# Performance work log

Measured on AMD Instinct MI355X. Metric: run time of the kernel, lower is better.

## Reference

```python
import math
import jax, jax.numpy as jnp
import numpy as np

B, S, D, H = 4, 2048, 1024, 16
HD = D // H
NEG = float(jnp.finfo(jnp.float16).min)  # matches torch.finfo(torch.float16).min

def setup_inputs() -> dict:
    key = jax.random.key(0)
    ks = jax.random.split(key, 10)
    s = 1.0 / math.sqrt(D)
    return {
        "x": jax.random.normal(ks[0], (B, S, D), jnp.float32),
        "mask": jax.random.randint(ks[1], (B, 1, S, S), 0, 2).astype(bool),
        "Wq": jax.random.normal(ks[2], (D, D), jnp.float32) * s,
        "bq": jnp.zeros((D,), jnp.float32),
        "Wk": jax.random.normal(ks[3], (D, D), jnp.float32) * s,
        "bk": jnp.zeros((D,), jnp.float32),
        "Wv": jax.random.normal(ks[4], (D, D), jnp.float32) * s,
        "bv": jnp.zeros((D,), jnp.float32),
        "Wf": jax.random.normal(ks[5], (D, D), jnp.float32) * s,
        "bf": jnp.zeros((D,), jnp.float32),
    }

def reference(x, mask, Wq, bq, Wk, bk, Wv, bv, Wf, bf):
    b, s, d = x.shape
    # QKV projections (torch Linear: y = x @ W.T + b)
    q = (x @ Wq.T + bq).reshape(b, s, H, HD).transpose(0, 2, 1, 3)  # [b,h,s,hd]
    k = (x @ Wk.T + bk).reshape(b, s, H, HD).transpose(0, 2, 1, 3)
    v = (x @ Wv.T + bv).reshape(b, s, H, HD).transpose(0, 2, 1, 3)
    scores = jnp.einsum('bhqd,bhkd->bhqk', q, k) / math.sqrt(HD)
    scores = jnp.where(mask, scores, NEG)  # masked_fill_(~mask, fp16 min)
    p = jax.nn.softmax(scores, axis=-1)    # dropout is identity (eval / drop_rate=0)
    h = jnp.einsum('bhqk,bhkd->bhqd', p, v).transpose(0, 2, 1, 3).reshape(b, s, d)
    return h @ Wf.T + bf
```

## Files before the change

### kernel.cpp

```cpp
#include <hip/hip_runtime.h>
#include <math.h>

constexpr int S = 2048, D = 1024, H = 16;
constexpr float QSCL = 0.18033688011112042f;

typedef __attribute__((ext_vector_type(8))) short bf16x8;
typedef __attribute__((ext_vector_type(4))) short s16x4;
typedef __attribute__((ext_vector_type(4))) float f32x4;
typedef __attribute__((ext_vector_type(16))) float f32x16;

#define MFMA16(a,b,c) __builtin_amdgcn_mfma_f32_16x16x32_bf16(a,b,c,0,0,0)
#define MFMA32(a,b,c) __builtin_amdgcn_mfma_f32_32x32x16_bf16(a,b,c,0,0,0)

#define GLDS16(g, l) __builtin_amdgcn_global_load_lds( \
    (const __attribute__((address_space(1))) unsigned*)(const void*)(g), \
    (__attribute__((address_space(3))) unsigned*)(void*)(l), 16, 0, 0)

__device__ inline short f2bf(float f) {
    union { float f; unsigned u; } c; c.f = f;
    unsigned u = c.u + 0x7fffu + ((c.u >> 16) & 1u);
    return (short)(u >> 16);
}

__global__ __launch_bounds__(256)
void conv_pack(const float* __restrict__ x,  const float* __restrict__ wq,
               const float* __restrict__ wk, const float* __restrict__ wv,
               const float* __restrict__ wf,
               short* __restrict__ xb,  short* __restrict__ wqb,
               short* __restrict__ wkb, short* __restrict__ wvb,
               short* __restrict__ wfb)
{
    int i = blockIdx.x * 256 + threadIdx.x;
    const float* s; short* d; int o;
    if (i < 2097152) { s = x; d = xb; o = i; }
    else {
        int j = i - 2097152; int wsel = j >> 18; o = j & 262143;
        s = wsel == 0 ? wq : wsel == 1 ? wk : wsel == 2 ? wv : wf;
        d = wsel == 0 ? wqb : wsel == 1 ? wkb : wsel == 2 ? wvb : wfb;
    }
    float4 v = ((const float4*)s)[o];
    s16x4 r; r.x = f2bf(v.x); r.y = f2bf(v.y); r.z = f2bf(v.z); r.w = f2bf(v.w);
    ((s16x4*)d)[o] = r;
}

__global__ __launch_bounds__(256)
void conv_maskcol(const int* __restrict__ m, unsigned* __restrict__ o)
{
    int gid = blockIdx.x * 256 + threadIdx.x;
    int lane = gid & 63;
    int tile = (gid >> 6) & 31;
    int grp  = (gid >> 11) & 63;
    int bb   = gid >> 17;
    int qrow = grp * 32 + (lane & 31);
    int h = lane >> 5;
    const int* base = m + (size_t)bb * S * S + (size_t)qrow * S + tile * 64 + 4 * h;
    unsigned wbits = 0;
#pragma unroll
    for (int a = 0; a < 8; ++a) {
        int4 v = *(const int4*)(base + 8 * (a & 3) + 32 * (a >> 2));
        wbits |= (v.x != 0 ? 1u : 0u) << (4 * a);
        wbits |= (v.y != 0 ? 1u : 0u) << (4 * a + 1);
        wbits |= (v.z != 0 ? 1u : 0u) << (4 * a + 2);
        wbits |= (v.w != 0 ? 1u : 0u) << (4 * a + 3);
    }
    o[gid] = wbits;
}

__global__ __launch_bounds__(256, 3)
void qkv_mfma(const short* __restrict__ xb, const short* __restrict__ wcat,
              const float* __restrict__ bq, const float* __restrict__ bk,
              const float* __restrict__ bv,
              short* __restrict__ qo, short* __restrict__ ko, short* __restrict__ vto)
{
    __shared__ short As[128 * 64];
    __shared__ short Bs[128 * 64];
    const int t = threadIdx.x, lane = t & 63;
    const int w = __builtin_amdgcn_readfirstlane(t >> 6);
    const int lr = lane & 15, lg = lane >> 4;
    const int wr = w >> 1, wc = w & 1;
    const int m0 = blockIdx.x * 128, n0 = blockIdx.y * 128;

    const int srow = t >> 3;
    const int scol = ((t & 7) ^ (srow & 7)) * 8;
    const short* asrc = xb   + (size_t)(m0 + srow) * 1024 + scol;
    const short* bsrc = wcat + (size_t)(n0 + srow) * 1024 + scol;
    char* aldst = (char*)As + w * 1024;
    char* bldst = (char*)Bs + w * 1024;

    f32x4 z = {0.f, 0.f, 0.f, 0.f};
    f32x4 acc[4][4];
#pragma unroll
    for (int i = 0; i < 4; ++i)
#pragma unroll
        for (int jj = 0; jj < 4; ++jj) acc[i][jj] = z;

    for (int kt = 0; kt < 1024; kt += 64) {
        __syncthreads();
        GLDS16(asrc + kt,             aldst);
        GLDS16(asrc + kt + 32 * 1024, aldst + 4096);
        GLDS16(asrc + kt + 64 * 1024, aldst + 8192);
        GLDS16(asrc + kt + 96 * 1024, aldst + 12288);
        GLDS16(bsrc + kt,             bldst);
        GLDS16(bsrc + kt + 32 * 1024, bldst + 4096);
        GLDS16(bsrc + kt + 64 * 1024, bldst + 8192);
        GLDS16(bsrc + kt + 96 * 1024, bldst + 12288);
        __syncthreads();
#pragma unroll
        for (int ks = 0; ks < 2; ++ks) {
            bf16x8 af[4], bfr[4];
#pragma unroll
            for (int fi = 0; fi < 4; ++fi) {
                const int ra = wr * 64 + fi * 16 + lr;
                af[fi] = *(const bf16x8*)((const char*)As + ra * 128 +
                          ((ks * 64 + lg * 16) ^ ((ra & 7) << 4)));
                const int rb = wc * 64 + fi * 16 + lr;
                bfr[fi] = *(const bf16x8*)((const char*)Bs + rb * 128 +
                          ((ks * 64 + lg * 16) ^ ((rb & 7) << 4)));
            }
#pragma unroll
            for (int fi = 0; fi < 4; ++fi)
#pragma unroll
                for (int fj = 0; fj < 4; ++fj)
                    acc[fi][fj] = MFMA16(af[fi], bfr[fj], acc[fi][fj]);
        }
    }

    const int bb = m0 >> 11;
    const int ssb = (m0 & (S - 1)) + wr * 64 + lg * 4;
    const int mat = n0 >> 10;
    const int nbase = (n0 & 1023) + wc * 64;

    if (mat == 0) {
#pragma unroll
        for (int fj = 0; fj < 4; ++fj) {
            const int nl = nbase + fj * 16 + lr, hh = nl >> 6, hd = nl & 63;
            const float bi = bq[nl];
#pragma unroll
            for (int fi = 0; fi < 4; ++fi)
#pragma unroll
                for (int r = 0; r < 4; ++r)
                    qo[(((size_t)bb * H + hh) * S + ssb + fi * 16 + r) * 64 + hd] =
                        f2bf((acc[fi][fj][r] + bi) * QSCL);
        }
    } else if (mat == 1) {
#pragma unroll
        for (int fj = 0; fj < 4; ++fj) {
            const int nl = nbase + fj * 16 + lr, hh = nl >> 6, hd = nl & 63;
            const float bi = bk[nl];
#pragma unroll
            for (int fi = 0; fi < 4; ++fi)
#pragma unroll
                for (int r = 0; r < 4; ++r)
                    ko[(((size_t)bb * H + hh) * S + ssb + fi * 16 + r) * 64 + hd] =
                        f2bf(acc[fi][fj][r] + bi);
        }
    } else {
#pragma unroll
        for (int fj = 0; fj < 4; ++fj) {
            const int nl = nbase + fj * 16 + lr, hh = nl >> 6, hd = nl & 63;
            const float bi = bv[nl];
#pragma unroll
            for (int fi = 0; fi < 4; ++fi) {
                s16x4 pk;
#pragma unroll
                for (int r = 0; r < 4; ++r) pk[r] = f2bf(acc[fi][fj][r] + bi);
                *(s16x4*)(vto + (((size_t)bb * H + hh) * 64 + hd) * S + ssb + fi * 16) = pk;
            }
        }
    }
}

__global__ __launch_bounds__(256, 3)
void attn_mfma4(const short* __restrict__ qg, const short* __restrict__ kg,
                const short* __restrict__ vtg,
                const unsigned* __restrict__ mcol,
                short* __restrict__ hc)
{
    __shared__ short Kl[2][64 * 64];
    __shared__ short Vl[2][64 * 64];

    const int t = threadIdx.x, lane = t & 63;
    const int w = __builtin_amdgcn_readfirstlane(t >> 6);
    const int l31 = lane & 31, h = lane >> 5;

    const int id = blockIdx.x;
    const int xcd = id & 7, j = id >> 3;
    const int bh = xcd + 8 * (j >> 4);
    const int q0 = (j & 15) * 128;
    const int bb = bh >> 4, hh = bh & 15;

    const short* qb  = qg  + (size_t)bh * S * 64;
    const short* kb  = kg  + (size_t)bh * S * 64;
    const short* vtb = vtg + (size_t)bh * 64 * S;
    const unsigned* mc = mcol + ((size_t)(bb * 64 + (q0 >> 5) + w)) * 32 * 64 + lane;

    const int qrow = q0 + w * 32 + l31;
    bf16x8 qf[4];
#pragma unroll
    for (int ds = 0; ds < 4; ++ds)
        qf[ds] = *(const bf16x8*)(qb + (size_t)qrow * 64 + ds * 16 + 8 * h);

    const int sk = t >> 3;
    const int soff = (((t & 7) * 16) ^ ((sk & 7) << 4)) >> 1;
    const int rbyte = l31 * 128;
    const int sz = (lane & 7) << 4;

    f32x16 z16;
#pragma unroll
    for (int i = 0; i < 16; ++i) z16[i] = 0.f;
    f32x16 O0 = z16, O1 = z16, Lacc = z16;

    bf16x8 ones;
#pragma unroll
    for (int i = 0; i < 8; ++i) ones[i] = (short)0x3F80;

    auto issue_stage = [&](int kt, int buf) {
        const short* ks0 = kb + (size_t)(kt + sk) * 64 + soff;
        const short* vs0 = vtb + (size_t)sk * S + kt + soff;
        char* kB = (char*)&Kl[buf][0] + w * 1024;
        char* vB = (char*)&Vl[buf][0] + w * 1024;
        GLDS16(ks0, kB);
        GLDS16(ks0 + 32 * 64, kB + 4096);
        GLDS16(vs0, vB);
        GLDS16(vs0 + (size_t)32 * S, vB + 4096);
    };

    issue_stage(0, 0);
    __syncthreads();

    for (int tile = 0; tile < 32; ++tile) {
        const int cur = tile & 1;
        if (tile < 31) issue_stage((tile + 1) * 64, cur ^ 1);
        const unsigned mcw = mc[tile * 64];

        f32x16 s0 = z16, s1 = z16;
        const char* Kb = (const char*)&Kl[cur][0];
#pragma unroll
        for (int ds = 0; ds < 4; ++ds) {
            const int off = ((ds * 32 + h * 16) ^ sz);
            bf16x8 a0 = *(const bf16x8*)(Kb + rbyte + off);
            bf16x8 a1 = *(const bf16x8*)(Kb + 4096 + rbyte + off);
            s0 = MFMA32(a0, qf[ds], s0);
            s1 = MFMA32(a1, qf[ds], s1);
        }

        const char* Vb = (const char*)&Vl[cur][0];
#pragma unroll
        for (int ks = 0; ks < 4; ++ks) {
            const int rb = (ks < 2) ? ks * 8 : (ks - 2) * 8;
            const int wb = (ks < 2) ? rb : 16 + rb;
            float pv[8];
#pragma unroll
            for (int jj = 0; jj < 8; ++jj) {
                float sv = (ks < 2) ? s0[rb + jj] : s1[rb + jj];
                sv = (mcw & (1u << (wb + jj))) ? sv : -INFINITY;
                pv[jj] = exp2f(sv);
            }
            int w0a, w1a, w0b, w1b;
            asm("v_cvt_pk_bf16_f32 %0, %1, %2" : "=v"(w0a) : "v"(pv[0]), "v"(pv[1]));
            asm("v_cvt_pk_bf16_f32 %0, %1, %2" : "=v"(w1a) : "v"(pv[2]), "v"(pv[3]));
            asm("v_cvt_pk_bf16_f32 %0, %1, %2" : "=v"(w0b) : "v"(pv[4]), "v"(pv[5]));
            asm("v_cvt_pk_bf16_f32 %0, %1, %2" : "=v"(w1b) : "v"(pv[6]), "v"(pv[7]));
            asm("v_permlane32_swap_b32 %0, %1" : "+v"(w0a), "+v"(w0b));
            asm("v_permlane32_swap_b32 %0, %1" : "+v"(w1a), "+v"(w1b));
            union { int i[4]; bf16x8 v; } pf;
            pf.i[0] = w0a; pf.i[1] = w1a; pf.i[2] = w0b; pf.i[3] = w1b;

            const int koff = ((ks * 32 + h * 16) ^ sz);
            bf16x8 v0 = *(const bf16x8*)(Vb + rbyte + koff);
            bf16x8 v1 = *(const bf16x8*)(Vb + 4096 + rbyte + koff);
            O0 = MFMA32(pf.v, v0, O0);
            O1 = MFMA32(pf.v, v1, O1);
            Lacc = MFMA32(pf.v, ones, Lacc);
        }
        __syncthreads();
    }

    const size_t outb = (size_t)bb * S * D + (size_t)hh * 64;
#pragma unroll
    for (int r = 0; r < 16; ++r) {
        const float inv = 1.f / Lacc[r];
        const int row = q0 + w * 32 + (r & 3) + 8 * (r >> 2) + 4 * h;
        hc[outb + (size_t)row * D + l31]      = f2bf(O0[r] * inv);
        hc[outb + (size_t)row * D + 32 + l31] = f2bf(O1[r] * inv);
    }
}

__global__ __launch_bounds__(256, 3)
void proj_mfma(const short* __restrict__ hb, const short* __restrict__ wfb,
               const float* __restrict__ bfp, float* __restrict__ out)
{
    __shared__ short As[128 * 64];
    __shared__ short Bs[128 * 64];
    const int t = threadIdx.x, lane = t & 63;
    const int w = __builtin_amdgcn_readfirstlane(t >> 6);
    const int lr = lane & 15, lg = lane >> 4;
    const int wr = w >> 1, wc = w & 1;
    const int m0 = blockIdx.x * 128, n0 = blockIdx.y * 128;

    const int srow = t >> 3;
    const int scol = ((t & 7) ^ (srow & 7)) * 8;
    const short* asrc = hb  + (size_t)(m0 + srow) * 1024 + scol;
    const short* bsrc = wfb + (size_t)(n0 + srow) * 1024 + scol;
    char* aldst = (char*)As + w * 1024;
    char* bldst = (char*)Bs + w * 1024;

    f32x4 z = {0.f, 0.f, 0.f, 0.f};
    f32x4 acc[4][4];
#pragma unroll
    for (int i = 0; i < 4; ++i)
#pragma unroll
        for (int jj = 0; jj < 4; ++jj) acc[i][jj] = z;

    for (int kt = 0; kt < 1024; kt += 64) {
        __syncthreads();
        GLDS16(asrc + kt,             aldst);
        GLDS16(asrc + kt + 32 * 1024, aldst + 4096);
        GLDS16(asrc + kt + 64 * 1024, aldst + 8192);
        GLDS16(asrc + kt + 96 * 1024, aldst + 12288);
        GLDS16(bsrc + kt,             bldst);
        GLDS16(bsrc + kt + 32 * 1024, bldst + 4096);
        GLDS16(bsrc + kt + 64 * 1024, bldst + 8192);
        GLDS16(bsrc + kt + 96 * 1024, bldst + 12288);
        __syncthreads();
#pragma unroll
        for (int ks = 0; ks < 2; ++ks) {
            bf16x8 af[4], bfr[4];
#pragma unroll
            for (int fi = 0; fi < 4; ++fi) {
                const int ra = wr * 64 + fi * 16 + lr;
                af[fi] = *(const bf16x8*)((const char*)As + ra * 128 +
                          ((ks * 64 + lg * 16) ^ ((ra & 7) << 4)));
                const int rb = wc * 64 + fi * 16 + lr;
                bfr[fi] = *(const bf16x8*)((const char*)Bs + rb * 128 +
                          ((ks * 64 + lg * 16) ^ ((rb & 7) << 4)));
            }
#pragma unroll
            for (int fi = 0; fi < 4; ++fi)
#pragma unroll
                for (int fj = 0; fj < 4; ++fj)
                    acc[fi][fj] = MFMA16(af[fi], bfr[fj], acc[fi][fj]);
        }
    }

#pragma unroll
    for (int fj = 0; fj < 4; ++fj) {
        const int nl = n0 + wc * 64 + fj * 16 + lr;
        const float bi = bfp[nl];
#pragma unroll
        for (int fi = 0; fi < 4; ++fi)
#pragma unroll
            for (int r = 0; r < 4; ++r)
                out[(size_t)(m0 + wr * 64 + fi * 16 + lg * 4 + r) * 1024 + nl] =
                    acc[fi][fj][r] + bi;
    }
}

extern "C" void kernel_launch(void* const* d_in, const int* in_sizes, int n_in,
                              void* d_out, int out_size, void* d_ws, size_t ws_size,
                              hipStream_t stream)
{
    const float* x  = (const float*)d_in[0];
    const int* mask = (const int*)d_in[1];
    const float* Wq = (const float*)d_in[2];
    const float* bq = (const float*)d_in[3];
    const float* Wk = (const float*)d_in[4];
    const float* bk = (const float*)d_in[5];
    const float* Wv = (const float*)d_in[6];
    const float* bv = (const float*)d_in[7];
    const float* Wf = (const float*)d_in[8];
    const float* bf = (const float*)d_in[9];
    float* out = (float*)d_out;

    char* p = (char*)d_ws;
    short* xb  = (short*)p; p += 16777216;
    short* wqb = (short*)p; p += 2097152;
    short* wkb = (short*)p; p += 2097152;
    short* wvb = (short*)p; p += 2097152;
    short* wfb = (short*)p; p += 2097152;
    unsigned* mcol = (unsigned*)p; p += 2097152;
    short* qb  = (short*)p; p += 16777216;
    short* kb  = (short*)p; p += 16777216;
    short* vtb = (short*)p; p += 16777216;
    short* hcb = (short*)p; p += 16777216;

    conv_pack<<<12288, 256, 0, stream>>>(x, Wq, Wk, Wv, Wf, xb, wqb, wkb, wvb, wfb);
    conv_maskcol<<<2048, 256, 0, stream>>>(mask, mcol);
    qkv_mfma<<<dim3(64, 24), 256, 0, stream>>>(xb, wqb, bq, bk, bv, qb, kb, vtb);
    attn_mfma4<<<1024, 256, 0, stream>>>(qb, kb, vtb, mcol, hcb);
    proj_mfma<<<dim3(64, 8), 256, 0, stream>>>(hcb, wfb, bf, out);
}
```

Baseline: 231.0 us.

## Fold mask into score accumulator via identity MFMA with precomputed bf16 bias fragments

Adds a mask preprocessing kernel that writes a bf16 additive bias (0 or a large negative) laid out in MFMA fragment order. The attention kernel then seeds the score accumulators by multiplying these fragments with an identity matrix, which removes the per-element bit test and select before exp2. It also switches to the raw hardware exp2 builtin. In exchange it adds four extra MFMAs and four global loads per tile, plus a 32MB mask buffer that the new kernel writes with strided, uncoalesced reads. The path is chosen at runtime only when the workspace is large enough.

```diff
diff --git a/kernel.cpp b/kernel.cpp
--- a/kernel.cpp
+++ b/kernel.cpp
@@ -11,6 +11,12 @@
 
 #define MFMA16(a,b,c) __builtin_amdgcn_mfma_f32_16x16x32_bf16(a,b,c,0,0,0)
 #define MFMA32(a,b,c) __builtin_amdgcn_mfma_f32_32x32x16_bf16(a,b,c,0,0,0)
+
+#if __has_builtin(__builtin_amdgcn_exp2f)
+#define EXP2(x) __builtin_amdgcn_exp2f(x)
+#else
+#define EXP2(x) exp2f(x)
+#endif
 
 #define GLDS16(g, l) __builtin_amdgcn_global_load_lds( \
     (const __attribute__((address_space(1))) unsigned*)(const void*)(g), \
@@ -64,6 +70,28 @@
         wbits |= (v.w != 0 ? 1u : 0u) << (4 * a + 3);
     }
     o[gid] = wbits;
+}
+
+__global__ __launch_bounds__(256)
+void conv_maskfrag(const int* __restrict__ m, short* __restrict__ o)
+{
+    int u = blockIdx.x * 4 + (threadIdx.x >> 6);
+    int l = threadIdx.x & 63;
+    int l31 = l & 31, h = l >> 5;
+    int kt = u & 63, qg = (u >> 6) & 63, bb = u >> 12;
+    int key = kt * 32 + l31;
+    const int* mb = m + (size_t)bb * S * S + key;
+    size_t ob = (size_t)u * 1024 + l * 8;
+#pragma unroll
+    for (int f = 0; f < 2; ++f) {
+        bf16x8 frag;
+#pragma unroll
+        for (int jj = 0; jj < 8; ++jj) {
+            int q = qg * 32 + f * 16 + 8 * h + jj;
+            frag[jj] = mb[(size_t)q * S] != 0 ? (short)0 : (short)0xC53B;
+        }
+        *(bf16x8*)(o + ob + f * 512) = frag;
+    }
 }
 
 __global__ __launch_bounds__(256, 3)
@@ -170,10 +198,12 @@
     }
 }
 
+template<int USEFRAG>
 __global__ __launch_bounds__(256, 3)
-void attn_mfma4(const short* __restrict__ qg, const short* __restrict__ kg,
+void attn_mfma5(const short* __restrict__ qg, const short* __restrict__ kg,
                 const short* __restrict__ vtg,
                 const unsigned* __restrict__ mcol,
+                const short* __restrict__ mfrag,
                 short* __restrict__ hc)
 {
     __shared__ short Kl[2][64 * 64];
@@ -192,13 +222,22 @@
     const short* qb  = qg  + (size_t)bh * S * 64;
     const short* kb  = kg  + (size_t)bh * S * 64;
     const short* vtb = vtg + (size_t)bh * 64 * S;
-    const unsigned* mc = mcol + ((size_t)(bb * 64 + (q0 >> 5) + w)) * 32 * 64 + lane;
+    const int bqg = bb * 64 + (q0 >> 5) + w;
+    const unsigned* mc = mcol + (size_t)bqg * 32 * 64 + lane;
+    const short* mfb = mfrag + (size_t)bqg * 65536 + lane * 8;
 
     const int qrow = q0 + w * 32 + l31;
     bf16x8 qf[4];
 #pragma unroll
     for (int ds = 0; ds < 4; ++ds)
         qf[ds] = *(const bf16x8*)(qb + (size_t)qrow * 64 + ds * 16 + 8 * h);
+
+    bf16x8 idB0, idB1;
+#pragma unroll
+    for (int jj = 0; jj < 8; ++jj) {
+        idB0[jj] = (8 * h + jj == l31)      ? (short)0x3F80 : (short)0;
+        idB1[jj] = (8 * h + jj + 16 == l31) ? (short)0x3F80 : (short)0;
+    }
 
     const int sk = t >> 3;
     const int soff = (((t & 7) * 16) ^ ((sk & 7) << 4)) >> 1;
@@ -231,9 +270,24 @@
     for (int tile = 0; tile < 32; ++tile) {
         const int cur = tile & 1;
         if (tile < 31) issue_stage((tile + 1) * 64, cur ^ 1);
-        const unsigned mcw = mc[tile * 64];
-
-        f32x16 s0 = z16, s1 = z16;
+
+        f32x16 s0, s1;
+        unsigned mcw = 0;
+        if (USEFRAG) {
+            const short* mfp = mfb + tile * 2048;
+            bf16x8 A0a = *(const bf16x8*)(mfp);
+            bf16x8 A0b = *(const bf16x8*)(mfp + 512);
+            bf16x8 A1a = *(const bf16x8*)(mfp + 1024);
+            bf16x8 A1b = *(const bf16x8*)(mfp + 1536);
+            s0 = MFMA32(A0a, idB0, z16);
+            s0 = MFMA32(A0b, idB1, s0);
+            s1 = MFMA32(A1a, idB0, z16);
+            s1 = MFMA32(A1b, idB1, s1);
+        } else {
+            s0 = z16; s1 = z16;
+            mcw = mc[tile * 64];
+        }
+
         const char* Kb = (const char*)&Kl[cur][0];
 #pragma unroll
         for (int ds = 0; ds < 4; ++ds) {
@@ -253,8 +307,9 @@
 #pragma unroll
             for (int jj = 0; jj < 8; ++jj) {
                 float sv = (ks < 2) ? s0[rb + jj] : s1[rb + jj];
-                sv = (mcw & (1u << (wb + jj))) ? sv : -INFINITY;
-                pv[jj] = exp2f(sv);
+                if (!USEFRAG)
+                    sv = (mcw & (1u << (wb + jj))) ? sv : -INFINITY;
+                pv[jj] = EXP2(sv);
             }
             int w0a, w1a, w0b, w1b;
             asm("v_cvt_pk_bf16_f32 %0, %1, %2" : "=v"(w0a) : "v"(pv[0]), "v"(pv[1]));
@@ -378,15 +433,24 @@
     short* wkb = (short*)p; p += 2097152;
     short* wvb = (short*)p; p += 2097152;
     short* wfb = (short*)p; p += 2097152;
-    unsigned* mcol = (unsigned*)p; p += 2097152;
     short* qb  = (short*)p; p += 16777216;
     short* kb  = (short*)p; p += 16777216;
     short* vtb = (short*)p; p += 16777216;
     short* hcb = (short*)p; p += 16777216;
+    unsigned* mcol = (unsigned*)p; p += 2097152;
+    short* mfrag = (short*)p; p += 33554432;
+    const size_t need_frag = (size_t)(p - (char*)d_ws);
+
+    const bool usefrag = ws_size >= need_frag;
 
     conv_pack<<<12288, 256, 0, stream>>>(x, Wq, Wk, Wv, Wf, xb, wqb, wkb, wvb, wfb);
-    conv_maskcol<<<2048, 256, 0, stream>>>(mask, mcol);
     qkv_mfma<<<dim3(64, 24), 256, 0, stream>>>(xb, wqb, bq, bk, bv, qb, kb, vtb);
-    attn_mfma4<<<1024, 256, 0, stream>>>(qb, kb, vtb, mcol, hcb);
+    if (usefrag) {
+        conv_maskfrag<<<4096, 256, 0, stream>>>(mask, mfrag);
+        attn_mfma5<1><<<1024, 256, 0, stream>>>(qb, kb, vtb, mcol, mfrag, hcb);
+    } else {
+        conv_maskcol<<<2048, 256, 0, stream>>>(mask, mcol);
+        attn_mfma5<0><<<1024, 256, 0, stream>>>(qb, kb, vtb, mcol, mfrag, hcb);
+    }
     proj_mfma<<<dim3(64, 8), 256, 0, stream>>>(hcb, wfb, bf, out);
 }
```

New measurement: 218.5 us. 1.06x faster.

## Replace MFMA row-sum with scalar accumulation, prefetch mask word, use native exp2

Applied to the files above, without the earlier changes.

In the attention kernel, the softmax denominator is no longer computed with an extra MFMA against a ones vector. Each lane now accumulates its exp values in a scalar, combines the two half-waves with a shuffle, and redistributes the reciprocals to output rows with readlane. The mask word for the next tile is loaded one iteration ahead, and exp2f is swapped for the raw hardware exp2 builtin. The goal is to drop a third of the PV-phase MFMAs and hide the mask load latency, at the cost of extra VALU adds and possible precision differences from the unguarded exp2.

```diff
diff --git a/kernel.cpp b/kernel.cpp
--- a/kernel.cpp
+++ b/kernel.cpp
@@ -11,6 +11,12 @@
 
 #define MFMA16(a,b,c) __builtin_amdgcn_mfma_f32_16x16x32_bf16(a,b,c,0,0,0)
 #define MFMA32(a,b,c) __builtin_amdgcn_mfma_f32_32x32x16_bf16(a,b,c,0,0,0)
+
+#if __has_builtin(__builtin_amdgcn_exp2f)
+#define EXP2(x) __builtin_amdgcn_exp2f(x)
+#else
+#define EXP2(x) exp2f(x)
+#endif
 
 #define GLDS16(g, l) __builtin_amdgcn_global_load_lds( \
     (const __attribute__((address_space(1))) unsigned*)(const void*)(g), \
@@ -171,7 +177,7 @@
 }
 
 __global__ __launch_bounds__(256, 3)
-void attn_mfma4(const short* __restrict__ qg, const short* __restrict__ kg,
+void attn_mfma8(const short* __restrict__ qg, const short* __restrict__ kg,
                 const short* __restrict__ vtg,
                 const unsigned* __restrict__ mcol,
                 short* __restrict__ hc)
@@ -208,11 +214,8 @@
     f32x16 z16;
 #pragma unroll
     for (int i = 0; i < 16; ++i) z16[i] = 0.f;
-    f32x16 O0 = z16, O1 = z16, Lacc = z16;
-
-    bf16x8 ones;
-#pragma unroll
-    for (int i = 0; i < 8; ++i) ones[i] = (short)0x3F80;
+    f32x16 O0 = z16, O1 = z16;
+    float li = 0.f;
 
     auto issue_stage = [&](int kt, int buf) {
         const short* ks0 = kb + (size_t)(kt + sk) * 64 + soff;
@@ -225,13 +228,17 @@
         GLDS16(vs0 + (size_t)32 * S, vB + 4096);
     };
 
+    unsigned mcw = mc[0];
     issue_stage(0, 0);
     __syncthreads();
 
     for (int tile = 0; tile < 32; ++tile) {
         const int cur = tile & 1;
-        if (tile < 31) issue_stage((tile + 1) * 64, cur ^ 1);
-        const unsigned mcw = mc[tile * 64];
+        unsigned mcn = 0;
+        if (tile < 31) {
+            issue_stage((tile + 1) * 64, cur ^ 1);
+            mcn = mc[(tile + 1) * 64];
+        }
 
         f32x16 s0 = z16, s1 = z16;
         const char* Kb = (const char*)&Kl[cur][0];
@@ -254,15 +261,16 @@
             for (int jj = 0; jj < 8; ++jj) {
                 float sv = (ks < 2) ? s0[rb + jj] : s1[rb + jj];
                 sv = (mcw & (1u << (wb + jj))) ? sv : -INFINITY;
-                pv[jj] = exp2f(sv);
+                pv[jj] = EXP2(sv);
+                li += pv[jj];
             }
             int w0a, w1a, w0b, w1b;
-            asm("v_cvt_pk_bf16_f32 %0, %1, %2" : "=v"(w0a) : "v"(pv[0]), "v"(pv[1]));
-            asm("v_cvt_pk_bf16_f32 %0, %1, %2" : "=v"(w1a) : "v"(pv[2]), "v"(pv[3]));
-            asm("v_cvt_pk_bf16_f32 %0, %1, %2" : "=v"(w0b) : "v"(pv[4]), "v"(pv[5]));
-            asm("v_cvt_pk_bf16_f32 %0, %1, %2" : "=v"(w1b) : "v"(pv[6]), "v"(pv[7]));
-            asm("v_permlane32_swap_b32 %0, %1" : "+v"(w0a), "+v"(w0b));
-            asm("v_permlane32_swap_b32 %0, %1" : "+v"(w1a), "+v"(w1b));
+            asm volatile("v_cvt_pk_bf16_f32 %0, %1, %2" : "=v"(w0a) : "v"(pv[0]), "v"(pv[1]));
+            asm volatile("v_cvt_pk_bf16_f32 %0, %1, %2" : "=v"(w1a) : "v"(pv[2]), "v"(pv[3]));
+            asm volatile("v_cvt_pk_bf16_f32 %0, %1, %2" : "=v"(w0b) : "v"(pv[4]), "v"(pv[5]));
+            asm volatile("v_cvt_pk_bf16_f32 %0, %1, %2" : "=v"(w1b) : "v"(pv[6]), "v"(pv[7]));
+            asm volatile("v_permlane32_swap_b32 %0, %1" : "+v"(w0a), "+v"(w0b));
+            asm volatile("v_permlane32_swap_b32 %0, %1" : "+v"(w1a), "+v"(w1b));
             union { int i[4]; bf16x8 v; } pf;
             pf.i[0] = w0a; pf.i[1] = w1a; pf.i[2] = w0b; pf.i[3] = w1b;
 
@@ -271,18 +279,26 @@
             bf16x8 v1 = *(const bf16x8*)(Vb + 4096 + rbyte + koff);
             O0 = MFMA32(pf.v, v0, O0);
             O1 = MFMA32(pf.v, v1, O1);
-            Lacc = MFMA32(pf.v, ones, Lacc);
-        }
+        }
+
+        if (tile < 31) mcw = mcn;
         __syncthreads();
     }
 
+    li += __shfl_xor(li, 32);
+    const float inv = 1.f / li;
+    const int ib = __builtin_bit_cast(int, inv);
     const size_t outb = (size_t)bb * S * D + (size_t)hh * 64;
 #pragma unroll
     for (int r = 0; r < 16; ++r) {
-        const float inv = 1.f / Lacc[r];
-        const int row = q0 + w * 32 + (r & 3) + 8 * (r >> 2) + 4 * h;
-        hc[outb + (size_t)row * D + l31]      = f2bf(O0[r] * inv);
-        hc[outb + (size_t)row * D + 32 + l31] = f2bf(O1[r] * inv);
+        const int qp = (r & 3) + 8 * (r >> 2);
+        const int vlo = __builtin_amdgcn_readlane(ib, qp);
+        const int vhi = __builtin_amdgcn_readlane(ib, qp + 4);
+        const float ir = h ? __builtin_bit_cast(float, vhi)
+                           : __builtin_bit_cast(float, vlo);
+        const int row = q0 + w * 32 + qp + 4 * h;
+        hc[outb + (size_t)row * D + l31]      = f2bf(O0[r] * ir);
+        hc[outb + (size_t)row * D + 32 + l31] = f2bf(O1[r] * ir);
     }
 }
 
@@ -378,15 +394,15 @@
     short* wkb = (short*)p; p += 2097152;
     short* wvb = (short*)p; p += 2097152;
     short* wfb = (short*)p; p += 2097152;
-    unsigned* mcol = (unsigned*)p; p += 2097152;
     short* qb  = (short*)p; p += 16777216;
     short* kb  = (short*)p; p += 16777216;
     short* vtb = (short*)p; p += 16777216;
     short* hcb = (short*)p; p += 16777216;
+    unsigned* mcol = (unsigned*)p; p += 2097152;
 
     conv_pack<<<12288, 256, 0, stream>>>(x, Wq, Wk, Wv, Wf, xb, wqb, wkb, wvb, wfb);
     conv_maskcol<<<2048, 256, 0, stream>>>(mask, mcol);
     qkv_mfma<<<dim3(64, 24), 256, 0, stream>>>(xb, wqb, bq, bk, bv, qb, kb, vtb);
-    attn_mfma4<<<1024, 256, 0, stream>>>(qb, kb, vtb, mcol, hcb);
+    attn_mfma8<<<1024, 256, 0, stream>>>(qb, kb, vtb, mcol, hcb);
     proj_mfma<<<dim3(64, 8), 256, 0, stream>>>(hcb, wfb, bf, out);
 }
```

Measured after the change: 195.0 us. 1.18x faster.
